# Kernel optimization log

Measured on AMD Instinct MI355X. Metric: run time of the kernel, lower is better.

Reference implementation:

```python
import jax, jax.numpy as jnp
import numpy as np

DIM = 768
HEADS = 12
DIM_HEAD = 64
ROPE_BASE = 8192.0
LN_EPS = 1e-5


def setup_inputs() -> dict:
    key = jax.random.key(0)
    k1, k2, k3, k4 = jax.random.split(key, 4)
    B, N = 4, 2048
    x = jax.random.normal(k1, (B, N, DIM), dtype=jnp.float32)
    # 2D (time, pitch) coordinates in [0, 64)
    coords = jax.random.uniform(k2, (B, N, 2), dtype=jnp.float32) * 64.0
    ln_gamma = jnp.ones((DIM,), dtype=jnp.float32)
    ln_beta = jnp.zeros((DIM,), dtype=jnp.float32)
    w_qkv = jax.random.normal(k3, (3 * HEADS * DIM_HEAD, DIM), dtype=jnp.float32) * (DIM ** -0.5)
    w_out = jax.random.normal(k4, (DIM, HEADS * DIM_HEAD), dtype=jnp.float32) * ((HEADS * DIM_HEAD) ** -0.5)
    return {"x": x, "coords": coords, "ln_gamma": ln_gamma, "ln_beta": ln_beta,
            "w_qkv": w_qkv, "w_out": w_out}


def _rotate(t, cos, sin):
    # t: [B,H,N,ad]; cos/sin: [B,1,N,ad//2]
    t1 = t[..., 0::2]
    t2 = t[..., 1::2]
    return jnp.concatenate([t1 * cos - t2 * sin, t1 * sin + t2 * cos], axis=-1)


def _axis_cos_sin(coord, axis_dim):
    # coord: [B,N] -> cos/sin: [B,1,N,axis_dim//2]
    half = axis_dim // 2
    exp = jnp.arange(half, dtype=jnp.float32) / half
    inv_freq = jnp.exp(-exp * jnp.log(jnp.float32(ROPE_BASE)))  # [half]
    freqs = coord[:, :, None] * inv_freq[None, None, :]  # [B,N,half]
    return jnp.cos(freqs)[:, None], jnp.sin(freqs)[:, None]


def reference(x, coords, ln_gamma, ln_beta, w_qkv, w_out):
    B, N, D = x.shape
    scale = DIM_HEAD ** -0.5

    # LayerNorm
    mu = jnp.mean(x, axis=-1, keepdims=True)
    var = jnp.mean((x - mu) ** 2, axis=-1, keepdims=True)
    xn = (x - mu) * jax.lax.rsqrt(var + LN_EPS) * ln_gamma + ln_beta

    # QKV projection: [B,N,3*H*dh]
    qkv = jnp.einsum('bnd,ed->bne', xn, w_qkv)
    q, k, v = jnp.split(qkv, 3, axis=-1)

    def to_heads(t):
        return t.reshape(B, N, HEADS, DIM_HEAD).transpose(0, 2, 1, 3)  # b h n d
    q, k, v = to_heads(q), to_heads(k), to_heads(v)

    # 2D axial RoPE: x-axis on dims [0:dh//2), y-axis on dims [dh//2:dh)
    half = DIM_HEAD // 2
    slices = [(0, (0, half)), (1, (half, DIM_HEAD))]
    for axis_idx, (lo, hi) in slices:
        cos, sin = _axis_cos_sin(coords[..., axis_idx], hi - lo)
        q = jnp.concatenate([q[..., :lo], _rotate(q[..., lo:hi], cos, sin), q[..., hi:]], axis=-1)
        k = jnp.concatenate([k[..., :lo], _rotate(k[..., lo:hi], cos, sin), k[..., hi:]], axis=-1)

    # Attention
    dots = jnp.einsum('bhnd,bhmd->bhnm', q, k) * scale
    attn = jax.nn.softmax(dots, axis=-1)
    out = jnp.einsum('bhnm,bhmd->bhnd', attn, v)
    out = out.transpose(0, 2, 1, 3).reshape(B, N, HEADS * DIM_HEAD)
    return jnp.einsum('bne,de->bnd', out, w_out)
```

## Files before the change

### kernel.cpp

```cpp
#include <hip/hip_runtime.h>

#define B_ 4
#define N_ 2048
#define D_ 768
#define H_ 12
#define DH_ 64
#define ROWS_ (B_*N_)
#define E3_ (3*D_)
#define NCVT_ 1152
#define NLN_  2048

typedef _Float16 f16;
typedef __attribute__((ext_vector_type(8))) _Float16 half8;
typedef __attribute__((ext_vector_type(4))) _Float16 half4;
typedef __attribute__((ext_vector_type(2))) _Float16 half2;
typedef __attribute__((ext_vector_type(4))) float floatx4;

__device__ __forceinline__ void gload_lds16(const void* g, void* lds){
  __builtin_amdgcn_global_load_lds(
      (const __attribute__((address_space(1))) unsigned int*)g,
      (__attribute__((address_space(3))) unsigned int*)lds, 16, 0, 0);
}

__global__ __launch_bounds__(256) void prep_kernel(
    const float* __restrict__ wqkv, f16* __restrict__ W16,
    const float* __restrict__ wout, f16* __restrict__ Wo16,
    const float* __restrict__ x, const float* __restrict__ g,
    const float* __restrict__ be, f16* __restrict__ xn,
    const float* __restrict__ coords, float* __restrict__ T){
  int bx = blockIdx.x, tid = threadIdx.x;
  if (bx < NCVT_){
    const int n8a = E3_*D_/8, n8b = D_*D_/8;
    int i = bx*256 + tid;
    const float* src; f16* dst; int j;
    if (i < n8a){ src = wqkv; dst = W16; j = i; }
    else { j = i - n8a; if (j >= n8b) return; src = wout; dst = Wo16; }
    float4 a = ((const float4*)src)[2*j];
    float4 b = ((const float4*)src)[2*j+1];
    half8 h;
    h[0]=(f16)a.x; h[1]=(f16)a.y; h[2]=(f16)a.z; h[3]=(f16)a.w;
    h[4]=(f16)b.x; h[5]=(f16)b.y; h[6]=(f16)b.z; h[7]=(f16)b.w;
    *(half8*)(dst + (size_t)j*8) = h;
  } else if (bx < NCVT_ + NLN_){
    int w = tid >> 6, lane = tid & 63;
    int row = (bx - NCVT_)*4 + w;
    const float* xr = x + (size_t)row * D_;
    int c = lane*4;
    float4 f0 = *(const float4*)(xr + c);
    float4 f1 = *(const float4*)(xr + c + 256);
    float4 f2 = *(const float4*)(xr + c + 512);
    float s  = (f0.x+f0.y+f0.z+f0.w) + (f1.x+f1.y+f1.z+f1.w) + (f2.x+f2.y+f2.z+f2.w);
    float ss = (f0.x*f0.x+f0.y*f0.y+f0.z*f0.z+f0.w*f0.w)
             + (f1.x*f1.x+f1.y*f1.y+f1.z*f1.z+f1.w*f1.w)
             + (f2.x*f2.x+f2.y*f2.y+f2.z*f2.z+f2.w*f2.w);
    #pragma unroll
    for(int off=1; off<64; off<<=1){
      s  += __shfl_xor(s,  off, 64);
      ss += __shfl_xor(ss, off, 64);
    }
    float mean = s * (1.0f/D_);
    float var  = ss * (1.0f/D_) - mean*mean;
    float rstd = rsqrtf(var + 1e-5f);
    f16* xo = xn + (size_t)row * D_;
    #pragma unroll
    for(int part=0; part<3; ++part){
      float4 v = part==0 ? f0 : (part==1 ? f1 : f2);
      float4 gg = *(const float4*)(g  + c + part*256);
      float4 bb = *(const float4*)(be + c + part*256);
      half4 o;
      o[0] = (f16)((v.x-mean)*rstd*gg.x + bb.x);
      o[1] = (f16)((v.y-mean)*rstd*gg.y + bb.y);
      o[2] = (f16)((v.z-mean)*rstd*gg.z + bb.z);
      o[3] = (f16)((v.w-mean)*rstd*gg.w + bb.w);
      *(half4*)(xo + c + part*256) = o;
    }
  } else {
    int i = (bx - NCVT_ - NLN_)*256 + tid;
    int token = i >> 5, ax = (i >> 4) & 1, m = i & 15;
    float coord = coords[(size_t)token*2 + ax];
    float fr = exp2f((float)m * (-13.0f/16.0f));
    float sn, cs;
    sincosf(coord * fr, &sn, &cs);
    T[(size_t)token*64 + ax*32 + m]      = cs;
    T[(size_t)token*64 + ax*32 + 16 + m] = sn;
  }
}

__global__ __launch_bounds__(256) void qkv_gemm(const f16* __restrict__ A,
    const f16* __restrict__ W, const float* __restrict__ T,
    f16* __restrict__ Q, f16* __restrict__ Kt, f16* __restrict__ VT){
  __shared__ __align__(16) char smem[128*136*2];
  f16* sA = (f16*)smem;
  f16* sB = (f16*)(smem + 16384);
  f16* sT = (f16*)smem;
  int tid = threadIdx.x;
  int wgid = blockIdx.x;
  int swz = (wgid & 7) * 144 + (wgid >> 3);
  int row_t = swz / 18;
  int e_t   = swz - row_t*18;
  int row0 = row_t * 128;
  int e0   = e_t * 128;
  int w = tid >> 6, lane = tid & 63, quad = lane >> 4, l15 = lane & 15;
  int wr = (w >> 1) * 64, wc = (w & 1) * 64;
  int r8 = lane >> 3;
  int sc16 = ((lane & 7) ^ r8) * 8;
  int sw = l15 & 7;
  floatx4 acc[4][4];
  #pragma unroll
  for(int i=0;i<4;++i)
    #pragma unroll
    for(int j=0;j<4;++j) acc[i][j] = (floatx4){0.f,0.f,0.f,0.f};

  for(int k0=0; k0<D_; k0+=64){
    __syncthreads();
    #pragma unroll
    for(int j=0;j<4;++j){
      int rr = j*32 + w*8 + r8;
      gload_lds16(A + (size_t)(row0+rr)*D_ + k0 + sc16, sA + (j*32 + w*8)*64);
      gload_lds16(W + (size_t)(e0 +rr)*D_ + k0 + sc16, sB + (j*32 + w*8)*64);
    }
    __syncthreads();
    #pragma unroll
    for(int kk=0;kk<2;++kk){
      half8 af[4], bf[4];
      #pragma unroll
      for(int mi=0;mi<4;++mi)
        af[mi] = *(const half8*)&sA[(wr + mi*16 + l15)*64 + (((kk*4 + quad) ^ sw) << 3)];
      #pragma unroll
      for(int ni=0;ni<4;++ni)
        bf[ni] = *(const half8*)&sB[(wc + ni*16 + l15)*64 + (((kk*4 + quad) ^ sw) << 3)];
      #pragma unroll
      for(int mi=0;mi<4;++mi)
        #pragma unroll
        for(int ni=0;ni<4;++ni)
          acc[mi][ni] = __builtin_amdgcn_mfma_f32_16x16x32_f16(af[mi], bf[ni], acc[mi][ni], 0, 0, 0);
    }
  }
  int part = e0 / D_;
  int erel = e0 % D_;
  if (part == 2){
    __syncthreads();
    #pragma unroll
    for(int mi=0;mi<4;++mi){
      int r = wr + mi*16 + quad*4;
      #pragma unroll
      for(int ni=0;ni<4;++ni){
        int c = wc + ni*16 + l15;
        #pragma unroll
        for(int reg=0;reg<4;++reg)
          sT[(size_t)(r+reg)*136 + c] = (f16)acc[mi][ni][reg];
      }
    }
    __syncthreads();
    int colT = tid >> 1;
    int nh   = (tid & 1) * 64;
    int h = erel/64 + (colT >> 6);
    int d = colT & 63;
    int rbase = row0 + nh;
    int b = rbase >> 11, n = rbase & 2047;
    f16 tmp[64];
    #pragma unroll
    for(int j=0;j<64;++j) tmp[j] = sT[(size_t)(nh + j)*136 + colT];
    f16* op = VT + (((size_t)b*H_ + h)*DH_ + d)*N_ + n;
    #pragma unroll
    for(int j=0;j<8;++j) *(half8*)(op + j*8) = *(half8*)&tmp[j*8];
    return;
  }
  __syncthreads();
  #pragma unroll
  for(int mi=0;mi<4;++mi){
    int r = wr + mi*16 + quad*4;
    #pragma unroll
    for(int ni=0;ni<4;++ni){
      int c = wc + ni*16 + l15;
      #pragma unroll
      for(int reg=0;reg<4;++reg)
        sT[(size_t)(r+reg)*136 + c] = (f16)acc[mi][ni][reg];
    }
  }
  __syncthreads();
  int r  = tid >> 1;
  int hh = tid & 1;
  int n_global = row0 + r;
  const float* tt = T + (size_t)n_global*64;
  float tv[64];
  #pragma unroll
  for(int j=0;j<16;++j) *(float4*)&tv[j*4] = *(const float4*)(tt + j*4);
  f16 v[64];
  #pragma unroll
  for(int j=0;j<8;++j) *(half8*)&v[j*8] = *(const half8*)&sT[(size_t)r*136 + hh*64 + j*8];
  f16 o[64];
  #pragma unroll
  for(int ax=0; ax<2; ++ax){
    #pragma unroll
    for(int m=0;m<16;++m){
      float cs = tv[ax*32 + m];
      float sn = tv[ax*32 + 16 + m];
      float t1 = (float)v[ax*32 + 2*m];
      float t2 = (float)v[ax*32 + 2*m + 1];
      o[ax*32 + m]      = (f16)(t1*cs - t2*sn);
      o[ax*32 + 16 + m] = (f16)(t1*sn + t2*cs);
    }
  }
  int h = erel/64 + hh;
  int b = n_global >> 11, n = n_global & 2047;
  f16* dst = (part==0) ? Q : Kt;
  f16* op = dst + (((size_t)b*H_ + h)*N_ + n)*DH_;
  #pragma unroll
  for(int j=0;j<8;++j) *(half8*)(op + j*8) = *(half8*)&o[j*8];
}

__global__ __launch_bounds__(256, 3) void attn_kernel(const f16* __restrict__ Q,
    const f16* __restrict__ K, const f16* __restrict__ VT, f16* __restrict__ AO){
  __shared__ f16 sK[2][64*64];
  __shared__ f16 sV[2][64*64];
  __shared__ f16 sP[4][2][16*64];
  int wgid = blockIdx.x;
  int swz = (wgid & 7) * 96 + (wgid >> 3);
  int bh = swz >> 4;
  int q0 = (swz & 15) * 128;
  int tid = threadIdx.x;
  int w = tid >> 6, lane = tid & 63, quad = lane >> 4, l15 = lane & 15;
  const f16* Qb = Q  + (size_t)bh*N_*DH_;
  const f16* Ks = K  + (size_t)bh*N_*DH_;
  const f16* Vb = VT + (size_t)bh*DH_*N_;

  int sd = tid >> 2, sc = tid & 3;
  const f16* vp = Vb + (size_t)sd*N_ + sc*16;
  const f16* kp = Ks + (size_t)sd*DH_ + sc*16;
  int sw0 = sd*64 + (((2*sc    ) ^ (sd & 7)) << 3);
  int sw1 = sd*64 + (((2*sc + 1) ^ (sd & 7)) << 3);

  half8 qf0[2], qf1[2];
  #pragma unroll
  for(int s2=0;s2<2;++s2){
    const f16* qrow = Qb + (size_t)(q0 + 32*w + 16*s2 + l15)*DH_ + quad*8;
    qf0[s2] = *(const half8*)(qrow);
    qf1[s2] = *(const half8*)(qrow + 32);
    half8 cs8;
    #pragma unroll
    for(int j=0;j<8;++j) cs8[j] = (f16)0.18033688f;
    qf0[s2] = qf0[s2] * cs8;
    qf1[s2] = qf1[s2] * cs8;
  }

  {
    half8 k0 = *(const half8*)(kp);
    half8 k1 = *(const half8*)(kp + 8);
    half8 g0 = *(const half8*)(vp);
    half8 g1 = *(const half8*)(vp + 8);
    *(half8*)&sK[0][sw0] = k0;  *(half8*)&sK[0][sw1] = k1;
    *(half8*)&sV[0][sw0] = g0;  *(half8*)&sV[0][sw1] = g1;
  }
  kp += 64*DH_;  vp += 64;

  float l_run[2] = {0.0f, 0.0f};
  floatx4 acc[2][4];
  #pragma unroll
  for(int s2=0;s2<2;++s2)
    #pragma unroll
    for(int dt=0;dt<4;++dt) acc[s2][dt] = (floatx4){0.f,0.f,0.f,0.f};
  __syncthreads();

  int sw = l15 & 7;
  f16* Prow[2] = { &sP[w][0][l15*64], &sP[w][1][l15*64] };

  const floatx4 SINIT = (floatx4){-8.f,-8.f,-8.f,-8.f};

#define ATTN_BODY(CUR, NXT) { \
    half8 nk0 = *(const half8*)(kp);      half8 nk1 = *(const half8*)(kp + 8); \
    half8 ng0 = *(const half8*)(vp);      half8 ng1 = *(const half8*)(vp + 8); \
    kp += 64*DH_;  vp += 64; \
    const f16* sk = &sK[CUR][0]; \
    half8 kf0[4], kf1[4]; \
    _Pragma("unroll") \
    for(int nt=0;nt<4;++nt){ \
      int rr = 16*nt + l15; \
      kf0[nt] = *(const half8*)&sk[rr*64 + ((quad       ^ sw) << 3)]; \
      kf1[nt] = *(const half8*)&sk[rr*64 + (((quad + 4) ^ sw) << 3)]; \
    } \
    floatx4 s_[2][4]; \
    _Pragma("unroll") \
    for(int s2=0;s2<2;++s2) \
      _Pragma("unroll") \
      for(int nt=0; nt<4; ++nt){ \
        floatx4 z = SINIT; \
        z = __builtin_amdgcn_mfma_f32_16x16x32_f16(kf0[nt], qf0[s2], z, 0, 0, 0); \
        z = __builtin_amdgcn_mfma_f32_16x16x32_f16(kf1[nt], qf1[s2], z, 0, 0, 0); \
        s_[s2][nt] = z; \
      } \
    _Pragma("unroll") \
    for(int s2=0;s2<2;++s2){ \
      f16* Pb = Prow[s2]; \
      float r4[4]; \
      _Pragma("unroll") \
      for(int nt=0;nt<4;++nt){ \
        float p0 = __builtin_amdgcn_exp2f(s_[s2][nt][0]); \
        float p1 = __builtin_amdgcn_exp2f(s_[s2][nt][1]); \
        float p2 = __builtin_amdgcn_exp2f(s_[s2][nt][2]); \
        float p3 = __builtin_amdgcn_exp2f(s_[s2][nt][3]); \
        auto lo_ = __builtin_amdgcn_cvt_pkrtz(p0, p1); \
        auto hi_ = __builtin_amdgcn_cvt_pkrtz(p2, p3); \
        half2 lo, hi; \
        __builtin_memcpy(&lo, &lo_, 4);  __builtin_memcpy(&hi, &hi_, 4); \
        half4 h = __builtin_shufflevector(lo, hi, 0, 1, 2, 3); \
        *(half4*)&Pb[(((2*nt + (quad>>1)) ^ sw) << 3) + ((quad & 1) << 2)] = h; \
        r4[nt] = (p0+p1)+(p2+p3); \
      } \
      l_run[s2] += (r4[0]+r4[1])+(r4[2]+r4[3]); \
    } \
    { \
      const f16* sv = &sV[CUR][0]; \
      half8 pf0a = *(const half8*)&Prow[0][((quad       ^ sw) << 3)]; \
      half8 pf1a = *(const half8*)&Prow[0][(((4 + quad) ^ sw) << 3)]; \
      half8 pf0b = *(const half8*)&Prow[1][((quad       ^ sw) << 3)]; \
      half8 pf1b = *(const half8*)&Prow[1][(((4 + quad) ^ sw) << 3)]; \
      _Pragma("unroll") \
      for(int dt=0;dt<4;++dt){ \
        int rr = 16*dt + l15; \
        half8 v0 = *(const half8*)&sv[rr*64 + ((quad       ^ sw) << 3)]; \
        half8 v1 = *(const half8*)&sv[rr*64 + (((quad + 4) ^ sw) << 3)]; \
        acc[0][dt] = __builtin_amdgcn_mfma_f32_16x16x32_f16(v0, pf0a, acc[0][dt], 0, 0, 0); \
        acc[0][dt] = __builtin_amdgcn_mfma_f32_16x16x32_f16(v1, pf1a, acc[0][dt], 0, 0, 0); \
        acc[1][dt] = __builtin_amdgcn_mfma_f32_16x16x32_f16(v0, pf0b, acc[1][dt], 0, 0, 0); \
        acc[1][dt] = __builtin_amdgcn_mfma_f32_16x16x32_f16(v1, pf1b, acc[1][dt], 0, 0, 0); \
      } \
    } \
    { \
      f16* dk = &sK[NXT][0]; \
      f16* dv = &sV[NXT][0]; \
      *(half8*)&dk[sw0] = nk0;  *(half8*)&dk[sw1] = nk1; \
      *(half8*)&dv[sw0] = ng0;  *(half8*)&dv[sw1] = ng1; \
    } \
    __syncthreads(); \
  }

  #pragma unroll 1
  for(int t=0; t<N_/128; ++t){
    ATTN_BODY(0, 1);
    ATTN_BODY(1, 0);
  }
#undef ATTN_BODY

  int b = bh / H_, h = bh % H_;
  #pragma unroll
  for(int s2=0;s2<2;++s2){
    float l = l_run[s2];
    l += __shfl_xor(l, 16, 64);
    l += __shfl_xor(l, 32, 64);
    float inv = 1.0f / l;
    f16* Pb = Prow[s2];
    #pragma unroll
    for(int dt=0;dt<4;++dt){
      half4 h4;
      h4[0]=(f16)(acc[s2][dt][0]*inv); h4[1]=(f16)(acc[s2][dt][1]*inv);
      h4[2]=(f16)(acc[s2][dt][2]*inv); h4[3]=(f16)(acc[s2][dt][3]*inv);
      *(half4*)&Pb[(((2*dt + (quad>>1)) ^ sw) << 3) + ((quad & 1) << 2)] = h4;
    }
    half8 o0 = *(const half8*)&Pb[(((2*quad    ) ^ sw) << 3)];
    half8 o1 = *(const half8*)&Pb[(((2*quad + 1) ^ sw) << 3)];
    f16* op = AO + ((size_t)(b*N_ + q0 + 32*w + 16*s2 + l15))*D_ + h*DH_ + quad*16;
    *(half8*)(op)     = o0;
    *(half8*)(op + 8) = o1;
  }
}

__global__ __launch_bounds__(256) void out_gemm(const f16* __restrict__ A,
    const f16* __restrict__ W, float* __restrict__ C){
  __shared__ f16 sA[128*64];
  __shared__ f16 sB[128*64];
  int tid = threadIdx.x;
  int wgid = blockIdx.x;
  int swz = (wgid & 7) * 48 + (wgid >> 3);
  int row_t = swz / 6;
  int e_t   = swz - row_t*6;
  int row0 = row_t * 128;
  int e0   = e_t * 128;
  int w = tid >> 6, lane = tid & 63, quad = lane >> 4, l15 = lane & 15;
  int wr = (w >> 1) * 64, wc = (w & 1) * 64;
  int r8 = lane >> 3;
  int sc16 = ((lane & 7) ^ r8) * 8;
  int sw = l15 & 7;
  floatx4 acc[4][4];
  #pragma unroll
  for(int i=0;i<4;++i)
    #pragma unroll
    for(int j=0;j<4;++j) acc[i][j] = (floatx4){0.f,0.f,0.f,0.f};

  for(int k0=0; k0<D_; k0+=64){
    __syncthreads();
    #pragma unroll
    for(int j=0;j<4;++j){
      int rr = j*32 + w*8 + r8;
      gload_lds16(A + (size_t)(row0+rr)*D_ + k0 + sc16, sA + (j*32 + w*8)*64);
      gload_lds16(W + (size_t)(e0 +rr)*D_ + k0 + sc16, sB + (j*32 + w*8)*64);
    }
    __syncthreads();
    #pragma unroll
    for(int kk=0;kk<2;++kk){
      half8 af[4], bf[4];
      #pragma unroll
      for(int mi=0;mi<4;++mi)
        af[mi] = *(const half8*)&sA[(wr + mi*16 + l15)*64 + (((kk*4 + quad) ^ sw) << 3)];
      #pragma unroll
      for(int ni=0;ni<4;++ni)
        bf[ni] = *(const half8*)&sB[(wc + ni*16 + l15)*64 + (((kk*4 + quad) ^ sw) << 3)];
      #pragma unroll
      for(int mi=0;mi<4;++mi)
        #pragma unroll
        for(int ni=0;ni<4;++ni)
          acc[mi][ni] = __builtin_amdgcn_mfma_f32_16x16x32_f16(af[mi], bf[ni], acc[mi][ni], 0, 0, 0);
    }
  }
  #pragma unroll
  for(int ni=0;ni<4;++ni){
    int col = e0 + wc + ni*16 + l15;
    #pragma unroll
    for(int mi=0;mi<4;++mi){
      int rbase = row0 + wr + mi*16 + quad*4;
      #pragma unroll
      for(int reg=0;reg<4;++reg)
        C[(size_t)(rbase+reg)*D_ + col] = acc[mi][ni][reg];
    }
  }
}

extern "C" void kernel_launch(void* const* d_in, const int* in_sizes, int n_in,
                              void* d_out, int out_size, void* d_ws, size_t ws_size,
                              hipStream_t stream) {
  (void)in_sizes; (void)n_in; (void)out_size; (void)ws_size;
  const float* x      = (const float*)d_in[0];
  const float* coords = (const float*)d_in[1];
  const float* g      = (const float*)d_in[2];
  const float* be     = (const float*)d_in[3];
  const float* wqkv   = (const float*)d_in[4];
  const float* wout   = (const float*)d_in[5];
  float* out = (float*)d_out;
  char* ws = (char*)d_ws;
  const size_t SEG = (size_t)ROWS_ * D_ * 2;
  f16* xn  = (f16*)(ws + 0*SEG);
  f16* Q   = (f16*)(ws + 1*SEG);
  f16* K   = (f16*)(ws + 2*SEG);
  f16* VT  = (f16*)(ws + 3*SEG);
  f16* AO  = (f16*)(ws + 4*SEG);
  f16* W16 = (f16*)(ws + 5*SEG);
  f16* Wo16= (f16*)(ws + 5*SEG + (size_t)E3_*D_*2);
  float* T = (float*)AO;

  prep_kernel<<<NCVT_ + NLN_ + 1024, 256, 0, stream>>>(
      wqkv, W16, wout, Wo16, x, g, be, xn, coords, T);
  qkv_gemm   <<<1152, 256, 0, stream>>>(xn, W16, T, Q, K, VT);
  attn_kernel<<<768, 256, 0, stream>>>(Q, K, VT, AO);
  out_gemm   <<<384, 256, 0, stream>>>(AO, Wo16, out);
}
```

Before: 237.0 us.

## Retile QKV GEMM to 256x128 with 8 waves, halve out GEMM tile rows

The QKV GEMM moves to 512-thread blocks covering 256x128 output tiles, so each W tile loaded into LDS is reused across twice as many rows. Its epilogue now writes V transposed straight from registers as half4 stores, and applies RoPE to Q/K in two half-width LDS passes so the staging buffer fits. The output GEMM switches to 64x128 tiles and doubles its grid, raising the block count for better CU occupancy on the smaller problem. The risks are the extra barriers in the two-pass epilogue, scattered 8-byte VT stores, and more redundant W loads in the out GEMM.

```diff
diff --git a/kernel.cpp b/kernel.cpp
--- a/kernel.cpp
+++ b/kernel.cpp
@@ -86,21 +86,21 @@
   }
 }
 
-__global__ __launch_bounds__(256) void qkv_gemm(const f16* __restrict__ A,
+__global__ __launch_bounds__(512, 4) void qkv_gemm(const f16* __restrict__ A,
     const f16* __restrict__ W, const float* __restrict__ T,
     f16* __restrict__ Q, f16* __restrict__ Kt, f16* __restrict__ VT){
-  __shared__ __align__(16) char smem[128*136*2];
+  __shared__ __align__(16) char smem[49152];
   f16* sA = (f16*)smem;
-  f16* sB = (f16*)(smem + 16384);
+  f16* sB = (f16*)(smem + 32768);
   f16* sT = (f16*)smem;
   int tid = threadIdx.x;
+  int w = tid >> 6, lane = tid & 63, quad = lane >> 4, l15 = lane & 15;
   int wgid = blockIdx.x;
-  int swz = (wgid & 7) * 144 + (wgid >> 3);
+  int swz = (wgid & 7) * 72 + (wgid >> 3);
   int row_t = swz / 18;
   int e_t   = swz - row_t*18;
-  int row0 = row_t * 128;
+  int row0 = row_t * 256;
   int e0   = e_t * 128;
-  int w = tid >> 6, lane = tid & 63, quad = lane >> 4, l15 = lane & 15;
   int wr = (w >> 1) * 64, wc = (w & 1) * 64;
   int r8 = lane >> 3;
   int sc16 = ((lane & 7) ^ r8) * 8;
@@ -114,11 +114,11 @@
   for(int k0=0; k0<D_; k0+=64){
     __syncthreads();
     #pragma unroll
-    for(int j=0;j<4;++j){
-      int rr = j*32 + w*8 + r8;
-      gload_lds16(A + (size_t)(row0+rr)*D_ + k0 + sc16, sA + (j*32 + w*8)*64);
-      gload_lds16(W + (size_t)(e0 +rr)*D_ + k0 + sc16, sB + (j*32 + w*8)*64);
-    }
+    for(int j=0;j<4;++j)
+      gload_lds16(A + (size_t)(row0 + j*64 + w*8 + r8)*D_ + k0 + sc16, sA + (j*64 + w*8)*64);
+    #pragma unroll
+    for(int j=0;j<2;++j)
+      gload_lds16(W + (size_t)(e0 + j*64 + w*8 + r8)*D_ + k0 + sc16, sB + (j*64 + w*8)*64);
     __syncthreads();
     #pragma unroll
     for(int kk=0;kk<2;++kk){
@@ -139,75 +139,69 @@
   int part = e0 / D_;
   int erel = e0 % D_;
   if (part == 2){
-    __syncthreads();
-    #pragma unroll
-    for(int mi=0;mi<4;++mi){
-      int r = wr + mi*16 + quad*4;
-      #pragma unroll
-      for(int ni=0;ni<4;++ni){
-        int c = wc + ni*16 + l15;
+    #pragma unroll
+    for(int ni=0;ni<4;++ni){
+      int col = erel + wc + ni*16 + l15;
+      int h = col >> 6, d = col & 63;
+      #pragma unroll
+      for(int mi=0;mi<4;++mi){
+        int rbase = row0 + wr + mi*16 + quad*4;
+        int b = rbase >> 11, n = rbase & 2047;
+        half4 h4;
         #pragma unroll
-        for(int reg=0;reg<4;++reg)
-          sT[(size_t)(r+reg)*136 + c] = (f16)acc[mi][ni][reg];
+        for(int reg=0;reg<4;++reg) h4[reg] = (f16)acc[mi][ni][reg];
+        *(half4*)&VT[(((size_t)b*H_ + h)*DH_ + d)*N_ + n] = h4;
       }
     }
-    __syncthreads();
-    int colT = tid >> 1;
-    int nh   = (tid & 1) * 64;
-    int h = erel/64 + (colT >> 6);
-    int d = colT & 63;
-    int rbase = row0 + nh;
-    int b = rbase >> 11, n = rbase & 2047;
-    f16 tmp[64];
-    #pragma unroll
-    for(int j=0;j<64;++j) tmp[j] = sT[(size_t)(nh + j)*136 + colT];
-    f16* op = VT + (((size_t)b*H_ + h)*DH_ + d)*N_ + n;
-    #pragma unroll
-    for(int j=0;j<8;++j) *(half8*)(op + j*8) = *(half8*)&tmp[j*8];
     return;
   }
-  __syncthreads();
-  #pragma unroll
-  for(int mi=0;mi<4;++mi){
-    int r = wr + mi*16 + quad*4;
-    #pragma unroll
-    for(int ni=0;ni<4;++ni){
-      int c = wc + ni*16 + l15;
-      #pragma unroll
-      for(int reg=0;reg<4;++reg)
-        sT[(size_t)(r+reg)*136 + c] = (f16)acc[mi][ni][reg];
-    }
-  }
-  __syncthreads();
-  int r  = tid >> 1;
-  int hh = tid & 1;
-  int n_global = row0 + r;
-  const float* tt = T + (size_t)n_global*64;
-  float tv[64];
-  #pragma unroll
-  for(int j=0;j<16;++j) *(float4*)&tv[j*4] = *(const float4*)(tt + j*4);
-  f16 v[64];
-  #pragma unroll
-  for(int j=0;j<8;++j) *(half8*)&v[j*8] = *(const half8*)&sT[(size_t)r*136 + hh*64 + j*8];
-  f16 o[64];
-  #pragma unroll
-  for(int ax=0; ax<2; ++ax){
-    #pragma unroll
-    for(int m=0;m<16;++m){
-      float cs = tv[ax*32 + m];
-      float sn = tv[ax*32 + 16 + m];
-      float t1 = (float)v[ax*32 + 2*m];
-      float t2 = (float)v[ax*32 + 2*m + 1];
-      o[ax*32 + m]      = (f16)(t1*cs - t2*sn);
-      o[ax*32 + 16 + m] = (f16)(t1*sn + t2*cs);
-    }
-  }
-  int h = erel/64 + hh;
-  int b = n_global >> 11, n = n_global & 2047;
   f16* dst = (part==0) ? Q : Kt;
-  f16* op = dst + (((size_t)b*H_ + h)*N_ + n)*DH_;
-  #pragma unroll
-  for(int j=0;j<8;++j) *(half8*)(op + j*8) = *(half8*)&o[j*8];
+  #pragma unroll 1
+  for(int pass=0; pass<2; ++pass){
+    __syncthreads();
+    if ((w & 1) == pass){
+      #pragma unroll
+      for(int mi=0;mi<4;++mi){
+        int r = wr + mi*16 + quad*4;
+        #pragma unroll
+        for(int ni=0;ni<4;++ni){
+          int c = ni*16 + l15;
+          #pragma unroll
+          for(int reg=0;reg<4;++reg)
+            sT[(size_t)(r+reg)*72 + c] = (f16)acc[mi][ni][reg];
+        }
+      }
+    }
+    __syncthreads();
+    int r  = tid >> 1;
+    int cc = tid & 1;
+    int n_global = row0 + r;
+    const float* tt = T + (size_t)n_global*64 + cc*32;
+    f16 v[32];
+    #pragma unroll
+    for(int j=0;j<4;++j) *(half8*)&v[j*8] = *(const half8*)&sT[(size_t)r*72 + cc*32 + j*8];
+    f16 o[32];
+    #pragma unroll
+    for(int mb=0;mb<4;++mb){
+      float4 cs4 = *(const float4*)(tt + mb*4);
+      float4 sn4 = *(const float4*)(tt + 16 + mb*4);
+      #pragma unroll
+      for(int mm=0;mm<4;++mm){
+        int m = mb*4 + mm;
+        float cs = ((const float*)&cs4)[mm];
+        float sn = ((const float*)&sn4)[mm];
+        float t1 = (float)v[2*m];
+        float t2 = (float)v[2*m + 1];
+        o[m]      = (f16)(t1*cs - t2*sn);
+        o[16 + m] = (f16)(t1*sn + t2*cs);
+      }
+    }
+    int h = erel/64 + pass;
+    int b = n_global >> 11, n = n_global & 2047;
+    f16* op = dst + (((size_t)b*H_ + h)*N_ + n)*DH_ + cc*32;
+    #pragma unroll
+    for(int j=0;j<4;++j) *(half8*)(op + j*8) = *(half8*)&o[j*8];
+  }
 }
 
 __global__ __launch_bounds__(256, 3) void attn_kernel(const f16* __restrict__ Q,
@@ -367,46 +361,46 @@
 
 __global__ __launch_bounds__(256) void out_gemm(const f16* __restrict__ A,
     const f16* __restrict__ W, float* __restrict__ C){
-  __shared__ f16 sA[128*64];
+  __shared__ f16 sA[64*64];
   __shared__ f16 sB[128*64];
   int tid = threadIdx.x;
   int wgid = blockIdx.x;
-  int swz = (wgid & 7) * 48 + (wgid >> 3);
+  int swz = (wgid & 7) * 96 + (wgid >> 3);
   int row_t = swz / 6;
   int e_t   = swz - row_t*6;
-  int row0 = row_t * 128;
+  int row0 = row_t * 64;
   int e0   = e_t * 128;
   int w = tid >> 6, lane = tid & 63, quad = lane >> 4, l15 = lane & 15;
-  int wr = (w >> 1) * 64, wc = (w & 1) * 64;
+  int wr = (w >> 1) * 32, wc = (w & 1) * 64;
   int r8 = lane >> 3;
   int sc16 = ((lane & 7) ^ r8) * 8;
   int sw = l15 & 7;
-  floatx4 acc[4][4];
-  #pragma unroll
-  for(int i=0;i<4;++i)
+  floatx4 acc[2][4];
+  #pragma unroll
+  for(int i=0;i<2;++i)
     #pragma unroll
     for(int j=0;j<4;++j) acc[i][j] = (floatx4){0.f,0.f,0.f,0.f};
 
   for(int k0=0; k0<D_; k0+=64){
     __syncthreads();
     #pragma unroll
-    for(int j=0;j<4;++j){
-      int rr = j*32 + w*8 + r8;
-      gload_lds16(A + (size_t)(row0+rr)*D_ + k0 + sc16, sA + (j*32 + w*8)*64);
-      gload_lds16(W + (size_t)(e0 +rr)*D_ + k0 + sc16, sB + (j*32 + w*8)*64);
-    }
+    for(int j=0;j<2;++j)
+      gload_lds16(A + (size_t)(row0 + j*32 + w*8 + r8)*D_ + k0 + sc16, sA + (j*32 + w*8)*64);
+    #pragma unroll
+    for(int j=0;j<4;++j)
+      gload_lds16(W + (size_t)(e0 + j*32 + w*8 + r8)*D_ + k0 + sc16, sB + (j*32 + w*8)*64);
     __syncthreads();
     #pragma unroll
     for(int kk=0;kk<2;++kk){
-      half8 af[4], bf[4];
-      #pragma unroll
-      for(int mi=0;mi<4;++mi)
+      half8 af[2], bf[4];
+      #pragma unroll
+      for(int mi=0;mi<2;++mi)
         af[mi] = *(const half8*)&sA[(wr + mi*16 + l15)*64 + (((kk*4 + quad) ^ sw) << 3)];
       #pragma unroll
       for(int ni=0;ni<4;++ni)
         bf[ni] = *(const half8*)&sB[(wc + ni*16 + l15)*64 + (((kk*4 + quad) ^ sw) << 3)];
       #pragma unroll
-      for(int mi=0;mi<4;++mi)
+      for(int mi=0;mi<2;++mi)
         #pragma unroll
         for(int ni=0;ni<4;++ni)
           acc[mi][ni] = __builtin_amdgcn_mfma_f32_16x16x32_f16(af[mi], bf[ni], acc[mi][ni], 0, 0, 0);
@@ -416,7 +410,7 @@
   for(int ni=0;ni<4;++ni){
     int col = e0 + wc + ni*16 + l15;
     #pragma unroll
-    for(int mi=0;mi<4;++mi){
+    for(int mi=0;mi<2;++mi){
       int rbase = row0 + wr + mi*16 + quad*4;
       #pragma unroll
       for(int reg=0;reg<4;++reg)
@@ -449,7 +443,7 @@
 
   prep_kernel<<<NCVT_ + NLN_ + 1024, 256, 0, stream>>>(
       wqkv, W16, wout, Wo16, x, g, be, xn, coords, T);
-  qkv_gemm   <<<1152, 256, 0, stream>>>(xn, W16, T, Q, K, VT);
+  qkv_gemm   <<<576, 512, 0, stream>>>(xn, W16, T, Q, K, VT);
   attn_kernel<<<768, 256, 0, stream>>>(Q, K, VT, AO);
-  out_gemm   <<<384, 256, 0, stream>>>(AO, Wo16, out);
-}
+  out_gemm   <<<768, 256, 0, stream>>>(AO, Wo16, out);
+}
```

After: 270.8 us. +14.2%, slower.
